# Kernel optimization log

Hardware: AMD Instinct MI355X
Metric: run time of the kernel (lower is better)

## Reference

```python
import jax, jax.numpy as jnp
import numpy as np

EMBED = 1024
HEADS = 16
HEAD_DIM = EMBED // HEADS
LN_EPS = 1e-5
XNORM_GAMMA = 0.01


def xnorm(x, gamma):
    # x * gamma / ||x||_4 along last dim (keepdim)
    norm4 = jnp.sum(x ** 4, axis=-1, keepdims=True) ** 0.25
    return x * gamma / norm4


def setup_inputs() -> dict:
    key = jax.random.key(0)
    ks = jax.random.split(key, 12)
    B, S = 2, 2048
    sc_hd = 1.0 / np.sqrt(HEAD_DIM)
    sc_e = 1.0 / np.sqrt(EMBED)
    return {
        "value": jax.random.normal(ks[0], (B, S, EMBED), jnp.float32),
        "key": jax.random.normal(ks[1], (B, S, EMBED), jnp.float32),
        "query": jax.random.normal(ks[2], (B, S, EMBED), jnp.float32),
        # per-head projections, torch Linear convention: y = x @ W.T
        "Wq": jax.random.normal(ks[3], (HEAD_DIM, HEAD_DIM), jnp.float32) * sc_hd,
        "Wk": jax.random.normal(ks[4], (HEAD_DIM, HEAD_DIM), jnp.float32) * sc_hd,
        "Wv": jax.random.normal(ks[5], (HEAD_DIM, HEAD_DIM), jnp.float32) * sc_hd,
        "Wo": jax.random.normal(ks[6], (EMBED, EMBED), jnp.float32) * sc_e,
        "bo": jnp.zeros((EMBED,), jnp.float32),
        "ln_w": jnp.ones((EMBED,), jnp.float32),
        "ln_b": jnp.zeros((EMBED,), jnp.float32),
        "Wsq": jax.random.normal(ks[7], (EMBED, EMBED), jnp.float32) * sc_e,
        "bsq": jnp.zeros((EMBED,), jnp.float32),
    }


def reference(value, key, query, Wq, Wk, Wv, Wo, bo, ln_w, ln_b, Wsq, bsq):
    B, S, E = query.shape
    # split heads: [B, S, H, D]
    v = value.reshape(B, S, HEADS, HEAD_DIM)
    k = key.reshape(B, S, HEADS, HEAD_DIM)
    q = query.reshape(B, S, HEADS, HEAD_DIM)
    v = jnp.einsum('nshd,ed->nshe', v, Wv)
    k = jnp.einsum('nshd,ed->nshe', k, Wk)
    q = jnp.einsum('nshd,ed->nshe', q, Wq)
    # energy: [B, H, Sq, Sk]
    energy = jnp.einsum('nqhd,nkhd->nhqk', q, k)
    energy_n = xnorm(energy, XNORM_GAMMA)
    v_n = xnorm(v, XNORM_GAMMA)
    out = jnp.einsum('nhql,nlhd->nqhd', energy_n, v_n).reshape(B, S, E)
    attn = out @ Wo.T + bo
    # LayerNorm(attention + query) over embed dim
    x = attn + query
    mu = jnp.mean(x, axis=-1, keepdims=True)
    var = jnp.mean((x - mu) ** 2, axis=-1, keepdims=True)
    x = (x - mu) / jnp.sqrt(var + LN_EPS) * ln_w + ln_b
    # SE gating: x * sigmoid(Linear(x))
    gate = jax.nn.sigmoid(x @ Wsq.T + bsq)
    return x * gate
```

## Files before the change

### kernel.cpp

```cpp
#include <hip/hip_runtime.h>
#include <stdint.h>

#define B_ 2
#define S_ 2048
#define E_ 1024
#define H_ 16
#define HD_ 64
#define N_ (B_*S_)
#define BH_ (B_*H_)
#define GAMMA 0.01f

typedef __attribute__((ext_vector_type(8))) short bf16x8;
typedef __attribute__((ext_vector_type(4))) float f32x4;
typedef __attribute__((ext_vector_type(2))) float f32x2;
typedef __attribute__((ext_vector_type(16))) float f32x16;
typedef unsigned short u16;
typedef unsigned int u32;

#define SWZ(row, kb) ((kb) ^ (((row)&7)<<4))

__device__ __forceinline__ u16 f2bf(float f){
  union { float f; u32 u; } v; v.f = f;
  return (u16)((v.u + 0x7FFFu + ((v.u>>16)&1u)) >> 16);
}

__device__ __forceinline__ float bf2f(u16 u){
  union { u32 u; float f; } v; v.u = ((u32)u)<<16; return v.f;
}

__device__ __forceinline__ u32 cvt_pk_bf16(float lo, float hi){
  u32 r; asm("v_cvt_pk_bf16_f32 %0, %1, %2" : "=v"(r) : "v"(lo), "v"(hi)); return r;
}

__device__ __forceinline__ uint4 pack8(float4 a, float4 b){
  uint4 r;
  r.x = cvt_pk_bf16(a.x, a.y);
  r.y = cvt_pk_bf16(a.z, a.w);
  r.z = cvt_pk_bf16(b.x, b.y);
  r.w = cvt_pk_bf16(b.z, b.w);
  return r;
}

__device__ __forceinline__ bf16x8 ldfrag(const unsigned char* base, int row, int kbyte){
  return *reinterpret_cast<const bf16x8*>(base + row*128 + SWZ(row, kbyte));
}

__device__ __forceinline__ void gl_lds16(const void* g, void* l){
  __builtin_amdgcn_global_load_lds(
      (const __attribute__((address_space(1))) unsigned int*)g,
      (__attribute__((address_space(3))) unsigned int*)l, 16, 0, 0);
}

__device__ __forceinline__ void proj_mfma(const unsigned char* X, const unsigned char* W,
                                          int wid, int l15, int g4, f32x4 acc[4])
{
  f32x4 z = {0.f,0.f,0.f,0.f};
  acc[0]=z; acc[1]=z; acc[2]=z; acc[3]=z;
  #pragma unroll
  for (int kk=0;kk<2;++kk){
    int kbyte = kk*64 + g4*16;
    bf16x8 a = ldfrag(X, wid*16 + l15, kbyte);
    #pragma unroll
    for (int t=0;t<4;++t){
      bf16x8 w = ldfrag(W, t*16 + l15, kbyte);
      acc[t] = __builtin_amdgcn_mfma_f32_16x16x32_bf16(a, w, acc[t], 0, 0, 0);
    }
  }
}

__global__ __launch_bounds__(256) void k_proj(
    const float* __restrict__ qin, const float* __restrict__ kin, const float* __restrict__ vin,
    const float* __restrict__ Wq, const float* __restrict__ Wk, const float* __restrict__ Wv,
    u16* __restrict__ qp, u16* __restrict__ kp, u16* __restrict__ kpT, u16* __restrict__ vnT,
    const float* __restrict__ Wo, const float* __restrict__ Wsq,
    u16* __restrict__ wo16, u16* __restrict__ wsq16)
{
  __shared__ alignas(16) unsigned char sm[49152];
  if (blockIdx.y >= H_){
    int cblk = (blockIdx.y - H_)*64 + blockIdx.x;
    int n4 = (E_*E_)/4;
    for (int i = cblk*256 + threadIdx.x; i < 2*n4; i += 128*256){
      const float4* src; ushort4* dst; int j;
      if (i < n4){ src=(const float4*)Wo;  dst=(ushort4*)wo16;  j=i; }
      else       { src=(const float4*)Wsq; dst=(ushort4*)wsq16; j=i-n4; }
      float4 v = src[j];
      ushort4 p; p.x=f2bf(v.x); p.y=f2bf(v.y); p.z=f2bf(v.z); p.w=f2bf(v.w);
      dst[j] = p;
    }
    return;
  }
  const int XQ=0, XK=8192, XV=16384, WQS=24576, WKS=32768, WVS=40960;
  int tid = threadIdx.x, lane = tid&63, wid = tid>>6;
  int l15 = lane&15, g4 = lane>>4;
  int tb = blockIdx.x*64;
  int h  = blockIdx.y;
  int b  = tb >> 11;
  int sbase = tb & 2047;
  int bh = b*H_ + h;

  {
    int rl = tid>>2;
    int d0 = (tid&3)*16;
    const float* xs[3] = { qin, kin, vin };
    const float* wsrc[3] = { Wq, Wk, Wv };
    const int xoff[3] = {XQ,XK,XV}, woff[3] = {WQS,WKS,WVS};
    #pragma unroll
    for (int m3=0;m3<3;++m3){
      const float4* gx = reinterpret_cast<const float4*>(xs[m3] + (size_t)(tb+rl)*E_ + h*HD_ + d0);
      float4 a=gx[0], bb=gx[1], c=gx[2], d=gx[3];
      *(uint4*)(sm + xoff[m3] + rl*128 + SWZ(rl, d0*2))    = pack8(a,bb);
      *(uint4*)(sm + xoff[m3] + rl*128 + SWZ(rl, d0*2+16)) = pack8(c,d);
      const float4* gw = reinterpret_cast<const float4*>(wsrc[m3] + rl*64 + d0);
      float4 e=gw[0], f=gw[1], g2=gw[2], h2=gw[3];
      *(uint4*)(sm + woff[m3] + rl*128 + SWZ(rl, d0*2))    = pack8(e,f);
      *(uint4*)(sm + woff[m3] + rl*128 + SWZ(rl, d0*2+16)) = pack8(g2,h2);
    }
  }
  __syncthreads();

  f32x4 qacc[4], kacc[4], vacc[4];
  proj_mfma(sm+XQ, sm+WQS, wid, l15, g4, qacc);
  proj_mfma(sm+XK, sm+WKS, wid, l15, g4, kacc);
  proj_mfma(sm+XV, sm+WVS, wid, l15, g4, vacc);

  {
    float p4r[4] = {0.f,0.f,0.f,0.f};
    #pragma unroll
    for (int t=0;t<4;++t)
      #pragma unroll
      for (int r=0;r<4;++r){ float e = vacc[t][r]; float e2 = e*e; p4r[r] += e2*e2; }
    #pragma unroll
    for (int r=0;r<4;++r){
      float p = p4r[r];
      p += __shfl_xor(p,1); p += __shfl_xor(p,2); p += __shfl_xor(p,4); p += __shfl_xor(p,8);
      p4r[r] = GAMMA / sqrtf(sqrtf(p));
    }
    #pragma unroll
    for (int t=0;t<4;++t)
      #pragma unroll
      for (int r=0;r<4;++r) vacc[t][r] *= p4r[r];
  }

  __syncthreads();

  #pragma unroll
  for (int t=0;t<4;++t){
    int dd = t*16 + l15;
    #pragma unroll
    for (int r=0;r<4;++r){
      int tokl = wid*16 + g4*4 + r;
      *(u16*)(sm + XQ + tokl*128 + SWZ(tokl, dd*2)) = f2bf(qacc[t][r]);
      *(u16*)(sm + XK + tokl*128 + SWZ(tokl, dd*2)) = f2bf(kacc[t][r]);
    }
    #pragma unroll
    for (int r=0;r<4;r+=2){
      int tokl = wid*16 + g4*4 + r;
      *(u32*)(sm + XV  + dd*128 + SWZ(dd, tokl*2)) = cvt_pk_bf16(vacc[t][r], vacc[t][r+1]);
      *(u32*)(sm + WQS + dd*128 + SWZ(dd, tokl*2)) = cvt_pk_bf16(kacc[t][r], kacc[t][r+1]);
    }
  }
  __syncthreads();

  {
    int rl = tid>>2; int c2 = tid&3;
    uint4 q0 = *(const uint4*)(sm + XQ + rl*128 + SWZ(rl, c2*32));
    uint4 q1 = *(const uint4*)(sm + XQ + rl*128 + SWZ(rl, c2*32+16));
    size_t qg = ((size_t)bh*S_ + sbase + rl)*HD_ + c2*16;
    *(uint4*)(qp + qg)     = q0;
    *(uint4*)(qp + qg + 8) = q1;
    uint4 k0 = *(const uint4*)(sm + XK + rl*128 + SWZ(rl, c2*32));
    uint4 k1 = *(const uint4*)(sm + XK + rl*128 + SWZ(rl, c2*32+16));
    *(uint4*)(kp + qg)     = k0;
    *(uint4*)(kp + qg + 8) = k1;
    size_t vg = ((size_t)bh*HD_ + rl)*S_ + sbase + c2*16;
    uint4 v0 = *(const uint4*)(sm + XV + rl*128 + SWZ(rl, c2*32));
    uint4 v1 = *(const uint4*)(sm + XV + rl*128 + SWZ(rl, c2*32+16));
    *(uint4*)(vnT + vg)     = v0;
    *(uint4*)(vnT + vg + 8) = v1;
    uint4 t0 = *(const uint4*)(sm + WQS + rl*128 + SWZ(rl, c2*32));
    uint4 t1 = *(const uint4*)(sm + WQS + rl*128 + SWZ(rl, c2*32+16));
    *(uint4*)(kpT + vg)     = t0;
    *(uint4*)(kpT + vg + 8) = t1;
  }
}

__global__ __launch_bounds__(256) void k_kv(
    const u16* __restrict__ kpT, const u16* __restrict__ vnT, float* __restrict__ part)
{
  __shared__ alignas(128) unsigned char sm[65536];
  char* smc = (char*)sm;
  int tid = threadIdx.x, lane = tid&63, wv = tid>>6;
  int l31 = lane&31, hi = lane>>5;
  int bh = blockIdx.x >> 3, ch = blockIdx.x & 7;
  const char* kt = (const char*)(kpT + (size_t)bh*HD_*S_ + ch*256);
  const char* vt = (const char*)(vnT + (size_t)bh*HD_*S_ + ch*256);

  #pragma unroll
  for (int c=0;c<8;++c){
    int off = wv*8192 + c*1024 + lane*16;
    int row = off>>9, sl = (off&511)>>4;
    int ssl = sl ^ (row&31);
    gl_lds16(kt + (size_t)row*S_*2 + ssl*16, smc + off);
    gl_lds16(vt + (size_t)row*S_*2 + ssl*16, smc + 32768 + off);
  }
  asm volatile("s_waitcnt vmcnt(0)" ::: "memory");
  __builtin_amdgcn_s_barrier();
  asm volatile("" ::: "memory");

  auto LD = [&](int mo, int row, int byte) -> bf16x8 {
    return *reinterpret_cast<const bf16x8*>(smc + mo + row*512 + (byte ^ ((row&31)<<4)));
  };

  f32x16 acc[2][2] = {{{}, {}}, {{}, {}}};
  #pragma unroll
  for (int it=0; it<4; ++it){
    int kb = wv*128 + it*32 + hi*16;
    bf16x8 ka0 = LD(0,     l31,    kb);
    bf16x8 ka1 = LD(0,     32+l31, kb);
    bf16x8 vb0 = LD(32768, l31,    kb);
    bf16x8 vb1 = LD(32768, 32+l31, kb);
    acc[0][0] = __builtin_amdgcn_mfma_f32_32x32x16_bf16(ka0, vb0, acc[0][0], 0,0,0);
    acc[0][1] = __builtin_amdgcn_mfma_f32_32x32x16_bf16(ka1, vb0, acc[0][1], 0,0,0);
    acc[1][0] = __builtin_amdgcn_mfma_f32_32x32x16_bf16(ka0, vb1, acc[1][0], 0,0,0);
    acc[1][1] = __builtin_amdgcn_mfma_f32_32x32x16_bf16(ka1, vb1, acc[1][1], 0,0,0);
  }

  float* dstw = part + ((size_t)blockIdx.x*4 + wv)*4096;
  #pragma unroll
  for (int eh=0;eh<2;++eh)
    #pragma unroll
    for (int dh=0;dh<2;++dh){
      float* d2 = dstw + ((eh*2+dh)*64 + lane)*16;
      #pragma unroll
      for (int r4=0;r4<4;++r4)
        *(float4*)(d2 + r4*4) = make_float4(acc[eh][dh][r4*4],acc[eh][dh][r4*4+1],
                                            acc[eh][dh][r4*4+2],acc[eh][dh][r4*4+3]);
    }
}

__global__ __launch_bounds__(256) void k_kvr(
    const float* __restrict__ part, u16* __restrict__ MT)
{
  int tid = threadIdx.x, lane = tid&63, quad = tid>>6;
  int l31 = lane&31, hi = lane>>5;
  int bh = blockIdx.x;
  float s[16] = {0,0,0,0,0,0,0,0,0,0,0,0,0,0,0,0};
  #pragma unroll 4
  for (int p=0;p<32;++p){
    const float* src = part + ((size_t)(bh*8 + (p>>2))*4 + (p&3))*4096 + (quad*64 + lane)*16;
    #pragma unroll
    for (int r4=0;r4<4;++r4){
      float4 t = *(const float4*)(src + r4*4);
      s[r4*4]+=t.x; s[r4*4+1]+=t.y; s[r4*4+2]+=t.z; s[r4*4+3]+=t.w;
    }
  }
  int eh = quad>>1, dh = quad&1;
  int e = eh*32 + l31;
  u16* dst = MT + (size_t)bh*4096 + e*64;
  #pragma unroll
  for (int r=0;r<16;r+=2){
    int d = dh*32 + (r&3) + 8*(r>>2) + 4*hi;
    *(u32*)(dst + d) = cvt_pk_bf16(s[r], s[r+1]);
  }
}

__global__ __launch_bounds__(256, 2) void k_attn(
    const u16* __restrict__ qp, const u16* __restrict__ kp,
    const u16* __restrict__ MT, u16* __restrict__ ao)
{
  __shared__ alignas(128) unsigned char sm[49152];
  __shared__ float px[256];
  char* smc = (char*)sm;
  int tid = threadIdx.x, lane = tid&63, wv = tid>>6;
  int l31 = lane&31, hi = lane>>5;
  int qi = wv>>1, kj = wv&1;
  int L = blockIdx.x;
  int xcd = L&7, iw = L>>3;
  int bh = xcd*4 + (iw>>4);
  int qx = iw&15;
  int qb = qx*128;
  int b = bh>>4, h = bh&15;
  const u16* Kb = kp + (size_t)bh*S_*HD_;
  const u16* Qb = qp + (size_t)bh*S_*HD_;
  int q0 = qb + qi*64;

  bf16x8 qf[2][4];
  #pragma unroll
  for (int f=0;f<2;++f)
    #pragma unroll
    for (int kk=0;kk<4;++kk)
      qf[f][kk] = *reinterpret_cast<const bf16x8*>(Qb + (size_t)(q0 + f*32 + l31)*HD_ + kk*16 + hi*8);

  f32x16 z16 = {};
  f32x2 p4a[2] = {{0.f,0.f},{0.f,0.f}};
  f32x2 p4b[2] = {{0.f,0.f},{0.f,0.f}};

  const char* kSrcC[4];
  #pragma unroll
  for (int c=0;c<4;++c){
    int rk = wv*32 + c*8 + (lane>>3);
    int ck = ((lane&7)*16) ^ ((rk&7)<<4);
    kSrcC[c] = (const char*)Kb + (size_t)rk*128 + ck;
  }

  auto STAGE_K = [&](int bsel, int kt){
    char* db = smc + bsel*16384 + wv*4096;
    #pragma unroll
    for (int c=0;c<4;++c) gl_lds16(kSrcC[c] + (size_t)kt*16384, db + c*1024);
  };

  auto P4ACC = [&](const f32x16& e, f32x2& pa){
    #pragma unroll
    for (int j=0;j<8;++j){
      f32x2 pr = {e[2*j], e[2*j+1]};
      f32x2 e2;
      asm("v_pk_mul_f32 %0, %1, %1" : "=v"(e2) : "v"(pr));
      asm("v_pk_fma_f32 %0, %1, %1, %0" : "+v"(pa) : "v"(e2));
    }
  };

  auto QK = [&](const unsigned char* K_, int s2, f32x16& E0, f32x16& E1){
    bf16x8 ka[4];
    #pragma unroll
    for (int kk=0;kk<4;++kk) ka[kk] = ldfrag(K_, kj*64 + s2*32 + l31, kk*32 + hi*16);
    E0 = z16; E1 = z16;
    __builtin_amdgcn_s_setprio(1);
    #pragma unroll
    for (int kk=0;kk<4;++kk){
      E0 = __builtin_amdgcn_mfma_f32_32x32x16_bf16(ka[kk], qf[0][kk], E0, 0,0,0);
      E1 = __builtin_amdgcn_mfma_f32_32x32x16_bf16(ka[kk], qf[1][kk], E1, 0,0,0);
    }
    __builtin_amdgcn_s_setprio(0);
  };

  const int NT = S_/128;
  STAGE_K(0, 0); STAGE_K(1, 1);

  f32x16 eA0, eA1, eB0, eB1;

  #pragma unroll 1
  for (int t=0; t<NT; ++t){
    if (t < NT-1) { asm volatile("s_waitcnt vmcnt(4)" ::: "memory"); }
    else          { asm volatile("s_waitcnt vmcnt(0)" ::: "memory"); }
    __builtin_amdgcn_s_barrier();
    asm volatile("" ::: "memory");
    if (t+2 < NT) STAGE_K((t+2)%3, t+2);

    const unsigned char* K_ = sm + (t%3)*16384;
    QK(K_, 0, eA0, eA1);
    QK(K_, 1, eB0, eB1);
    P4ACC(eA0, p4a[0]);
    P4ACC(eA1, p4a[1]);
    P4ACC(eB0, p4b[0]);
    P4ACC(eB1, p4b[1]);
  }

  float p4f[2];
  #pragma unroll
  for (int f=0;f<2;++f){
    p4f[f] = p4a[f].x + p4a[f].y + p4b[f].x + p4b[f].y;
    p4f[f] += __shfl_xor(p4f[f], 32);
  }
  __syncthreads();
  if (hi==0){
    px[((qi*2+0)*2+kj)*32 + l31] = p4f[0];
    px[((qi*2+1)*2+kj)*32 + l31] = p4f[1];
  }
  __syncthreads();
  #pragma unroll
  for (int f=0;f<2;++f) p4f[f] += px[((qi*2+f)*2+(1-kj))*32 + l31];
  float sc0 = GAMMA * rsqrtf(sqrtf(p4f[0]));
  float sc1 = GAMMA * rsqrtf(sqrtf(p4f[1]));

  const u16* mtb = MT + (size_t)bh*4096;
  bf16x8 mtf[4];
  #pragma unroll
  for (int kk=0;kk<4;++kk)
    mtf[kk] = *reinterpret_cast<const bf16x8*>(mtb + (kj*32 + l31)*64 + kk*16 + hi*8);
  f32x16 oA0 = z16, oA1 = z16;
  #pragma unroll
  for (int kk=0;kk<4;++kk){
    oA0 = __builtin_amdgcn_mfma_f32_32x32x16_bf16(mtf[kk], qf[0][kk], oA0, 0,0,0);
    oA1 = __builtin_amdgcn_mfma_f32_32x32x16_bf16(mtf[kk], qf[1][kk], oA1, 0,0,0);
  }

  __syncthreads();
  #pragma unroll
  for (int r=0;r<16;r+=2){
    int e = kj*32 + (r&3) + 8*(r>>2) + 4*hi;
    int ql0 = qi*64 + l31;
    *(u32*)(smc + ql0*128 + SWZ(ql0, e*2)) = cvt_pk_bf16(oA0[r]*sc0, oA0[r+1]*sc0);
    int ql1 = qi*64 + 32 + l31;
    *(u32*)(smc + ql1*128 + SWZ(ql1, e*2)) = cvt_pk_bf16(oA1[r]*sc1, oA1[r+1]*sc1);
  }
  __syncthreads();
  {
    int row = tid>>1, eh = tid&1;
    u16* dst = ao + ((size_t)b*S_ + qb + row)*E_ + h*HD_ + eh*32;
    #pragma unroll
    for (int c=0;c<4;++c)
      *(uint4*)(dst + c*8) = *(const uint4*)(smc + row*128 + SWZ(row, eh*64 + c*16));
  }
}

template<int MODE>
__global__ __launch_bounds__(256, 2) void k_gemm(
    const u16* __restrict__ A, const u16* __restrict__ Bw,
    const float* __restrict__ bias, const float* __restrict__ auxf,
    const u16* __restrict__ aux16, float* __restrict__ out32, u16* __restrict__ out16)
{
  __shared__ alignas(128) unsigned char sm[65536];
  char* smc = (char*)sm;
  int tid = threadIdx.x, lane = tid&63, wv = tid>>6;
  int l31 = lane&31, hi = lane>>5;
  int wr = wv>>1, wc = wv&1;
  int LL = (blockIdx.x & 7)*32 + (blockIdx.x >> 3);
  int mt = LL >> 3, nt = LL & 7;
  int m0 = mt*128, n0 = nt*128;

  const char* aS[4]; const char* bS[4];
  #pragma unroll
  for (int c=0;c<4;++c){
    int off = wv*4096 + c*1024 + lane*16;
    int r = off>>7, cl = off&127;
    int cs = cl ^ ((r&7)<<4);
    aS[c] = (const char*)A  + ((size_t)(m0+r)*E_)*2 + cs;
    bS[c] = (const char*)Bw + ((size_t)(n0+r)*E_)*2 + cs;
  }

  auto STAGE = [&](int bsel, int t){
    char* db = smc + bsel*32768 + wv*4096;
    size_t kb2 = (size_t)t*128;
    #pragma unroll
    for (int c=0;c<4;++c) gl_lds16(aS[c] + kb2, db + c*1024);
    #pragma unroll
    for (int c=0;c<4;++c) gl_lds16(bS[c] + kb2, db + 16384 + c*1024);
  };

  f32x16 acc[2][2] = {{{}, {}}, {{}, {}}};

  const int NK = E_/64;
  STAGE(0, 0); STAGE(1, 1);

  #pragma unroll 1
  for (int t=0; t<NK; ++t){
    if (t < NK-1) { asm volatile("s_waitcnt vmcnt(8)" ::: "memory"); }
    else          { asm volatile("s_waitcnt vmcnt(0)" ::: "memory"); }
    __builtin_amdgcn_s_barrier();
    asm volatile("" ::: "memory");

    const unsigned char* Ap_ = sm + (t&1)*32768;
    const unsigned char* Bp_ = Ap_ + 16384;
    #pragma unroll
    for (int kk=0;kk<4;++kk){
      int kbyte = kk*32 + hi*16;
      bf16x8 a0 = ldfrag(Ap_, wr*64 + l31,      kbyte);
      bf16x8 a1 = ldfrag(Ap_, wr*64 + 32 + l31, kbyte);
      bf16x8 b0 = ldfrag(Bp_, wc*64 + l31,      kbyte);
      bf16x8 b1 = ldfrag(Bp_, wc*64 + 32 + l31, kbyte);
      __builtin_amdgcn_s_setprio(1);
      acc[0][0] = __builtin_amdgcn_mfma_f32_32x32x16_bf16(a0, b0, acc[0][0], 0,0,0);
      acc[0][1] = __builtin_amdgcn_mfma_f32_32x32x16_bf16(a0, b1, acc[0][1], 0,0,0);
      acc[1][0] = __builtin_amdgcn_mfma_f32_32x32x16_bf16(a1, b0, acc[1][0], 0,0,0);
      acc[1][1] = __builtin_amdgcn_mfma_f32_32x32x16_bf16(a1, b1, acc[1][1], 0,0,0);
      __builtin_amdgcn_s_setprio(0);
    }

    asm volatile("" ::: "memory");
    __builtin_amdgcn_s_barrier();
    asm volatile("" ::: "memory");
    if (t+2 < NK) STAGE(t&1, t+2);
  }

  #pragma unroll
  for (int cg=0;cg<2;++cg){
    int col = n0 + wc*64 + cg*32 + l31;
    float bi = bias[col];
    #pragma unroll
    for (int rg=0;rg<2;++rg)
      #pragma unroll
      for (int r=0;r<16;++r){
        int mrow = m0 + wr*64 + rg*32 + (r&3) + 8*(r>>2) + 4*hi;
        size_t idx = (size_t)mrow*E_ + col;
        float v = acc[rg][cg][r] + bi;
        if (MODE == 0){
          out16[idx] = f2bf(v + auxf[idx]);
        } else {
          float gg = 1.f/(1.f + __expf(-v));
          out32[idx] = bf2f(aux16[idx]) * gg;
        }
      }
  }
}

__global__ __launch_bounds__(256) void k_ln(
    const u16* __restrict__ xin, const float* __restrict__ lnw, const float* __restrict__ lnb,
    u16* __restrict__ xout)
{
  __shared__ float red[8];
  __shared__ float stats[2];
  int row = blockIdx.x, tid = threadIdx.x;
  ushort4 xr = reinterpret_cast<const ushort4*>(xin + (size_t)row*E_)[tid];
  float x0 = bf2f(xr.x), x1 = bf2f(xr.y), x2 = bf2f(xr.z), x3 = bf2f(xr.w);
  float s  = x0 + x1 + x2 + x3;
  float s2 = x0*x0 + x1*x1 + x2*x2 + x3*x3;
  #pragma unroll
  for (int m=1;m<64;m<<=1){ s += __shfl_xor(s,m); s2 += __shfl_xor(s2,m); }
  if ((tid&63)==0){ red[tid>>6] = s; red[4+(tid>>6)] = s2; }
  __syncthreads();
  if (tid==0){
    float ts  = red[0]+red[1]+red[2]+red[3];
    float ts2 = red[4]+red[5]+red[6]+red[7];
    float mu  = ts * (1.f/E_);
    float var = ts2 * (1.f/E_) - mu*mu;
    stats[0] = mu; stats[1] = rsqrtf(var + 1e-5f);
  }
  __syncthreads();
  float mu = stats[0], rstd = stats[1];
  float4 w  = reinterpret_cast<const float4*>(lnw)[tid];
  float4 bb = reinterpret_cast<const float4*>(lnb)[tid];
  ushort4 p;
  p.x = f2bf((x0-mu)*rstd*w.x + bb.x);
  p.y = f2bf((x1-mu)*rstd*w.y + bb.y);
  p.z = f2bf((x2-mu)*rstd*w.z + bb.z);
  p.w = f2bf((x3-mu)*rstd*w.w + bb.w);
  reinterpret_cast<ushort4*>(xout + (size_t)row*E_)[tid] = p;
}

extern "C" void kernel_launch(void* const* d_in, const int* in_sizes, int n_in,
                              void* d_out, int out_size, void* d_ws, size_t ws_size,
                              hipStream_t stream)
{
  const float* value = (const float*)d_in[0];
  const float* key   = (const float*)d_in[1];
  const float* query = (const float*)d_in[2];
  const float* Wq    = (const float*)d_in[3];
  const float* Wk    = (const float*)d_in[4];
  const float* Wv    = (const float*)d_in[5];
  const float* Wo    = (const float*)d_in[6];
  const float* bo    = (const float*)d_in[7];
  const float* lnw   = (const float*)d_in[8];
  const float* lnb   = (const float*)d_in[9];
  const float* Wsq   = (const float*)d_in[10];
  const float* bsq   = (const float*)d_in[11];
  float* out = (float*)d_out;

  char* ws = (char*)d_ws;
  const size_t MB = 1ull<<20;
  u16*   qp     = (u16*)(ws + 0*MB);
  u16*   kp     = (u16*)(ws + 8*MB);
  u16*   vnT    = (u16*)(ws + 16*MB);
  u16*   kpT    = (u16*)(ws + 24*MB);
  u16*   ao     = (u16*)(ws + 32*MB);
  u16*   mtw    = (u16*)(ws + 44*MB);
  u16*   xres16 = (u16*)(ws + 8*MB);
  u16*   x16    = (u16*)(ws + 16*MB);
  float* part   = (float*)(ws + 64*MB);
  u16*   wo16   = (u16*)(ws + 48*MB);
  u16*   wsq16  = (u16*)(ws + 50*MB);

  k_proj<<<dim3(N_/64, H_+2), 256, 0, stream>>>(query, key, value, Wq, Wk, Wv,
                                                qp, kp, kpT, vnT, Wo, Wsq, wo16, wsq16);
  k_kv  <<<256, 256, 0, stream>>>(kpT, vnT, part);
  k_kvr <<<BH_, 256, 0, stream>>>(part, mtw);
  k_attn<<<512, 256, 0, stream>>>(qp, kp, mtw, ao);
  k_gemm<0><<<256, 256, 0, stream>>>(ao, wo16, bo, query, (const u16*)nullptr, (float*)nullptr, xres16);
  k_ln  <<<N_, 256, 0, stream>>>(xres16, lnw, lnb, x16);
  k_gemm<1><<<256, 256, 0, stream>>>(x16, wsq16, bsq, (const float*)nullptr, x16, out, (u16*)nullptr);
}
```

Before: 111.1 us.

## Retile attention kernel to 64-query blocks with double-buffered K and higher occupancy

The attention norm kernel now handles 64 queries per block instead of 128, and each of the four waves covers a distinct 32-key slice rather than a 2x2 query/key split. The grid doubles to 1024 blocks and launch bounds rise to 4 blocks per CU. The K staging changes from a triple buffer to a double buffer, which lowers LDS use to 32KB but adds a second barrier per iteration. The intent is more latency hiding through occupancy, at the cost of reloading K twice as often overall and extra synchronisation.

```diff
diff --git a/kernel.cpp b/kernel.cpp
--- a/kernel.cpp
+++ b/kernel.cpp
@@ -264,47 +264,43 @@
   }
 }
 
-__global__ __launch_bounds__(256, 2) void k_attn(
+__global__ __launch_bounds__(256, 4) void k_attn(
     const u16* __restrict__ qp, const u16* __restrict__ kp,
     const u16* __restrict__ MT, u16* __restrict__ ao)
 {
-  __shared__ alignas(128) unsigned char sm[49152];
-  __shared__ float px[256];
+  __shared__ alignas(128) unsigned char sm[32768];
+  __shared__ float px[4][2][32];
   char* smc = (char*)sm;
-  int tid = threadIdx.x, lane = tid&63, wv = tid>>6;
+  int tid = threadIdx.x, lane = tid&63, kj = tid>>6;
   int l31 = lane&31, hi = lane>>5;
-  int qi = wv>>1, kj = wv&1;
   int L = blockIdx.x;
   int xcd = L&7, iw = L>>3;
-  int bh = xcd*4 + (iw>>4);
-  int qx = iw&15;
-  int qb = qx*128;
+  int bh = xcd*4 + (iw>>5);
+  int qx = iw&31;
+  int qb = qx*64;
   int b = bh>>4, h = bh&15;
   const u16* Kb = kp + (size_t)bh*S_*HD_;
   const u16* Qb = qp + (size_t)bh*S_*HD_;
-  int q0 = qb + qi*64;
 
   bf16x8 qf[2][4];
   #pragma unroll
   for (int f=0;f<2;++f)
     #pragma unroll
     for (int kk=0;kk<4;++kk)
-      qf[f][kk] = *reinterpret_cast<const bf16x8*>(Qb + (size_t)(q0 + f*32 + l31)*HD_ + kk*16 + hi*8);
+      qf[f][kk] = *reinterpret_cast<const bf16x8*>(Qb + (size_t)(qb + f*32 + l31)*HD_ + kk*16 + hi*8);
 
   f32x16 z16 = {};
   f32x2 p4a[2] = {{0.f,0.f},{0.f,0.f}};
-  f32x2 p4b[2] = {{0.f,0.f},{0.f,0.f}};
 
   const char* kSrcC[4];
   #pragma unroll
   for (int c=0;c<4;++c){
-    int rk = wv*32 + c*8 + (lane>>3);
+    int rk = kj*32 + c*8 + (lane>>3);
     int ck = ((lane&7)*16) ^ ((rk&7)<<4);
     kSrcC[c] = (const char*)Kb + (size_t)rk*128 + ck;
   }
-
   auto STAGE_K = [&](int bsel, int kt){
-    char* db = smc + bsel*16384 + wv*4096;
+    char* db = smc + bsel*16384 + kj*4096;
     #pragma unroll
     for (int c=0;c<4;++c) gl_lds16(kSrcC[c] + (size_t)kt*16384, db + c*1024);
   };
@@ -319,24 +315,8 @@
     }
   };
 
-  auto QK = [&](const unsigned char* K_, int s2, f32x16& E0, f32x16& E1){
-    bf16x8 ka[4];
-    #pragma unroll
-    for (int kk=0;kk<4;++kk) ka[kk] = ldfrag(K_, kj*64 + s2*32 + l31, kk*32 + hi*16);
-    E0 = z16; E1 = z16;
-    __builtin_amdgcn_s_setprio(1);
-    #pragma unroll
-    for (int kk=0;kk<4;++kk){
-      E0 = __builtin_amdgcn_mfma_f32_32x32x16_bf16(ka[kk], qf[0][kk], E0, 0,0,0);
-      E1 = __builtin_amdgcn_mfma_f32_32x32x16_bf16(ka[kk], qf[1][kk], E1, 0,0,0);
-    }
-    __builtin_amdgcn_s_setprio(0);
-  };
-
   const int NT = S_/128;
   STAGE_K(0, 0); STAGE_K(1, 1);
-
-  f32x16 eA0, eA1, eB0, eB1;
 
   #pragma unroll 1
   for (int t=0; t<NT; ++t){
@@ -344,62 +324,69 @@
     else          { asm volatile("s_waitcnt vmcnt(0)" ::: "memory"); }
     __builtin_amdgcn_s_barrier();
     asm volatile("" ::: "memory");
-    if (t+2 < NT) STAGE_K((t+2)%3, t+2);
-
-    const unsigned char* K_ = sm + (t%3)*16384;
-    QK(K_, 0, eA0, eA1);
-    QK(K_, 1, eB0, eB1);
-    P4ACC(eA0, p4a[0]);
-    P4ACC(eA1, p4a[1]);
-    P4ACC(eB0, p4b[0]);
-    P4ACC(eB1, p4b[1]);
+    const unsigned char* K_ = sm + (t&1)*16384;
+
+    bf16x8 ka[4];
+    #pragma unroll
+    for (int kk=0;kk<4;++kk) ka[kk] = ldfrag(K_, kj*32 + l31, kk*32 + hi*16);
+    f32x16 e0 = z16, e1 = z16;
+    __builtin_amdgcn_s_setprio(1);
+    #pragma unroll
+    for (int kk=0;kk<4;++kk){
+      e0 = __builtin_amdgcn_mfma_f32_32x32x16_bf16(ka[kk], qf[0][kk], e0, 0,0,0);
+      e1 = __builtin_amdgcn_mfma_f32_32x32x16_bf16(ka[kk], qf[1][kk], e1, 0,0,0);
+    }
+    __builtin_amdgcn_s_setprio(0);
+    P4ACC(e0, p4a[0]);
+    P4ACC(e1, p4a[1]);
+
+    asm volatile("" ::: "memory");
+    __builtin_amdgcn_s_barrier();
+    asm volatile("" ::: "memory");
+    if (t+2 < NT) STAGE_K(t&1, t+2);
   }
 
   float p4f[2];
   #pragma unroll
   for (int f=0;f<2;++f){
-    p4f[f] = p4a[f].x + p4a[f].y + p4b[f].x + p4b[f].y;
+    p4f[f] = p4a[f].x + p4a[f].y;
     p4f[f] += __shfl_xor(p4f[f], 32);
   }
-  __syncthreads();
-  if (hi==0){
-    px[((qi*2+0)*2+kj)*32 + l31] = p4f[0];
-    px[((qi*2+1)*2+kj)*32 + l31] = p4f[1];
-  }
-  __syncthreads();
-  #pragma unroll
-  for (int f=0;f<2;++f) p4f[f] += px[((qi*2+f)*2+(1-kj))*32 + l31];
-  float sc0 = GAMMA * rsqrtf(sqrtf(p4f[0]));
-  float sc1 = GAMMA * rsqrtf(sqrtf(p4f[1]));
-
-  const u16* mtb = MT + (size_t)bh*4096;
-  bf16x8 mtf[4];
-  #pragma unroll
-  for (int kk=0;kk<4;++kk)
-    mtf[kk] = *reinterpret_cast<const bf16x8*>(mtb + (kj*32 + l31)*64 + kk*16 + hi*8);
-  f32x16 oA0 = z16, oA1 = z16;
-  #pragma unroll
-  for (int kk=0;kk<4;++kk){
-    oA0 = __builtin_amdgcn_mfma_f32_32x32x16_bf16(mtf[kk], qf[0][kk], oA0, 0,0,0);
-    oA1 = __builtin_amdgcn_mfma_f32_32x32x16_bf16(mtf[kk], qf[1][kk], oA1, 0,0,0);
-  }
-
-  __syncthreads();
-  #pragma unroll
-  for (int r=0;r<16;r+=2){
-    int e = kj*32 + (r&3) + 8*(r>>2) + 4*hi;
-    int ql0 = qi*64 + l31;
-    *(u32*)(smc + ql0*128 + SWZ(ql0, e*2)) = cvt_pk_bf16(oA0[r]*sc0, oA0[r+1]*sc0);
-    int ql1 = qi*64 + 32 + l31;
-    *(u32*)(smc + ql1*128 + SWZ(ql1, e*2)) = cvt_pk_bf16(oA1[r]*sc1, oA1[r+1]*sc1);
-  }
-  __syncthreads();
+  if (hi==0){ px[kj][0][l31] = p4f[0]; px[kj][1][l31] = p4f[1]; }
+  __syncthreads();
+  float sc0, sc1;
   {
-    int row = tid>>1, eh = tid&1;
-    u16* dst = ao + ((size_t)b*S_ + qb + row)*E_ + h*HD_ + eh*32;
-    #pragma unroll
-    for (int c=0;c<4;++c)
-      *(uint4*)(dst + c*8) = *(const uint4*)(smc + row*128 + SWZ(row, eh*64 + c*16));
+    float t0 = px[0][0][l31]+px[1][0][l31]+px[2][0][l31]+px[3][0][l31];
+    float t1 = px[0][1][l31]+px[1][1][l31]+px[2][1][l31]+px[3][1][l31];
+    sc0 = GAMMA * rsqrtf(sqrtf(t0));
+    sc1 = GAMMA * rsqrtf(sqrtf(t1));
+  }
+
+  if (kj < 2){
+    const u16* mtb = MT + (size_t)bh*4096;
+    bf16x8 mtf[4];
+    #pragma unroll
+    for (int kk=0;kk<4;++kk)
+      mtf[kk] = *reinterpret_cast<const bf16x8*>(mtb + (kj*32 + l31)*64 + kk*16 + hi*8);
+    f32x16 oA0 = z16, oA1 = z16;
+    #pragma unroll
+    for (int kk=0;kk<4;++kk){
+      oA0 = __builtin_amdgcn_mfma_f32_32x32x16_bf16(mtf[kk], qf[0][kk], oA0, 0,0,0);
+      oA1 = __builtin_amdgcn_mfma_f32_32x32x16_bf16(mtf[kk], qf[1][kk], oA1, 0,0,0);
+    }
+    #pragma unroll
+    for (int r=0;r<16;r+=2){
+      int e = kj*32 + (r&3) + 8*(r>>2) + 4*hi;
+      *(u32*)(smc + l31*128      + SWZ(l31,      e*2)) = cvt_pk_bf16(oA0[r]*sc0, oA0[r+1]*sc0);
+      *(u32*)(smc + (32+l31)*128 + SWZ(32+l31,   e*2)) = cvt_pk_bf16(oA1[r]*sc1, oA1[r+1]*sc1);
+    }
+  }
+  __syncthreads();
+  {
+    int row = tid>>2, c2 = tid&3;
+    u16* dst = ao + ((size_t)b*S_ + qb + row)*E_ + h*HD_ + c2*16;
+    *(uint4*)dst       = *(const uint4*)(smc + row*128 + SWZ(row, c2*32));
+    *(uint4*)(dst + 8) = *(const uint4*)(smc + row*128 + SWZ(row, c2*32+16));
   }
 }
 
@@ -563,7 +550,7 @@
                                                 qp, kp, kpT, vnT, Wo, Wsq, wo16, wsq16);
   k_kv  <<<256, 256, 0, stream>>>(kpT, vnT, part);
   k_kvr <<<BH_, 256, 0, stream>>>(part, mtw);
-  k_attn<<<512, 256, 0, stream>>>(qp, kp, mtw, ao);
+  k_attn<<<1024, 256, 0, stream>>>(qp, kp, mtw, ao);
   k_gemm<0><<<256, 256, 0, stream>>>(ao, wo16, bo, query, (const u16*)nullptr, (float*)nullptr, xres16);
   k_ln  <<<N_, 256, 0, stream>>>(xres16, lnw, lnb, x16);
   k_gemm<1><<<256, 256, 0, stream>>>(x16, wsq16, bsq, (const float*)nullptr, x16, out, (u16*)nullptr);
```

New measurement: 110.6 us. About the same (-0.5%).
